# Kernel optimization log

Hardware: AMD Instinct MI355X
Metric: run time of the kernel (lower is better)

The kernel has to match this reference:

```python
import jax, jax.numpy as jnp
import numpy as np

ROUTING_ITER = 3
EPS = 1e-8


def squash(caps, axis=-1, eps=EPS):
    dot = jnp.sum(caps * caps, axis=axis, keepdims=True)
    scale = dot / (1.0 + dot) / jnp.sqrt(dot + eps)
    return scale * caps


def setup_inputs() -> dict:
    key = jax.random.key(0)
    k1, k2, k3 = jax.random.split(key, 3)
    B, I, O, D_in, D_out = 32, 1024, 64, 16, 32
    x = jax.random.normal(k1, (B, I, D_in), dtype=jnp.float32)
    W = jax.random.normal(k2, (1, I, O, D_out, D_in), dtype=jnp.float32) * 0.05
    b = jax.random.normal(k3, (1, 1, O, D_out), dtype=jnp.float32) * 0.05
    return {"x": x, "W": W, "b": b}


def reference(x, W, b):
    # u_hat[b,i,o,d] = sum_n W[0,i,o,d,n] * x[b,i,n]
    u_hat = jnp.einsum('iodn,bin->biod', W[0], x)  # [B, I, O, D_out]
    u_hat_det = jax.lax.stop_gradient(u_hat)
    B, I, O, _ = u_hat.shape
    b_ij = jnp.zeros((B, I, O, 1), dtype=x.dtype)
    v_j = None
    for it in range(ROUTING_ITER):
        c_ij = jax.nn.softmax(b_ij, axis=2)  # over output capsules
        if it == ROUTING_ITER - 1:
            s_j = jnp.sum(c_ij * u_hat, axis=1, keepdims=True) + b  # [B,1,O,D]
            v_j = squash(s_j, axis=-1)
        else:
            s_j = jnp.sum(c_ij * u_hat_det, axis=1, keepdims=True)
            v_j = squash(s_j, axis=-1)
            a_ij = jnp.sum(u_hat_det * v_j, axis=-1, keepdims=True)  # agreement
            b_ij = b_ij + a_ij
    return jnp.squeeze(v_j)  # [B, O, D_out]
```

## Files before the change

### kernel.cpp

```cpp
#include <hip/hip_runtime.h>
#include <hip/hip_bf16.h>
#include <stdint.h>

#define B_  32
#define I_  1024
#define O_  64
#define D_  32
#define N_  16
#define OD_ 2048

__device__ __forceinline__ uint32_t f2bf1(float f) {
  uint32_t u = __float_as_uint(f);
  return (u + 0x7fffu + ((u >> 16) & 1u)) >> 16;
}
__device__ __forceinline__ uint32_t pack2(float a, float b) {
  return f2bf1(a) | (f2bf1(b) << 16);
}
__device__ __forceinline__ float bflo(uint32_t v) { return __uint_as_float(v << 16); }
__device__ __forceinline__ float bfhi(uint32_t v) { return __uint_as_float(v & 0xffff0000u); }
__device__ __forceinline__ void unpack8(uint4 r, float* u) {
  u[0] = bflo(r.x); u[1] = bfhi(r.x);
  u[2] = bflo(r.y); u[3] = bfhi(r.y);
  u[4] = bflo(r.z); u[5] = bfhi(r.z);
  u[6] = bflo(r.w); u[7] = bfhi(r.w);
}

__global__ __launch_bounds__(256) void k_einsum(const float* __restrict__ x,
                                                const float* __restrict__ W,
                                                uint16_t* __restrict__ uhat) {
  const int i = blockIdx.x >> 2;
  const int q = blockIdx.x & 3;
  const int t = threadIdx.x;
  const int od0 = q * 512 + t;
  __shared__ float xs[B_ * N_];
  for (int e = t; e < B_ * N_; e += 256) {
    int bb = e >> 4, n = e & 15;
    xs[e] = x[(size_t)bb * (I_ * N_) + (size_t)i * N_ + n];
  }
  float wA[16], wB[16];
  {
    const float4* Wa = (const float4*)(W + (size_t)i * (OD_ * N_) + (size_t)od0 * N_);
    const float4* Wb = (const float4*)(W + (size_t)i * (OD_ * N_) + (size_t)(od0 + 256) * N_);
    #pragma unroll
    for (int qq = 0; qq < 4; ++qq) {
      float4 fa = Wa[qq];
      wA[qq * 4 + 0] = fa.x; wA[qq * 4 + 1] = fa.y;
      wA[qq * 4 + 2] = fa.z; wA[qq * 4 + 3] = fa.w;
      float4 fb = Wb[qq];
      wB[qq * 4 + 0] = fb.x; wB[qq * 4 + 1] = fb.y;
      wB[qq * 4 + 2] = fb.z; wB[qq * 4 + 3] = fb.w;
    }
  }
  __syncthreads();
  #pragma unroll 2
  for (int bb = 0; bb < B_; ++bb) {
    float4 x0 = ((const float4*)(xs + bb * 16))[0];
    float4 x1 = ((const float4*)(xs + bb * 16))[1];
    float4 x2 = ((const float4*)(xs + bb * 16))[2];
    float4 x3 = ((const float4*)(xs + bb * 16))[3];
    float xv[16] = {x0.x, x0.y, x0.z, x0.w, x1.x, x1.y, x1.z, x1.w,
                    x2.x, x2.y, x2.z, x2.w, x3.x, x3.y, x3.z, x3.w};
    float a0 = 0.f, a1 = 0.f;
    #pragma unroll
    for (int n = 0; n < 16; ++n) {
      a0 = fmaf(wA[n], xv[n], a0);
      a1 = fmaf(wB[n], xv[n], a1);
    }
    const size_t base = ((size_t)bb * I_ + i) * OD_ + od0;
    uhat[base]       = (uint16_t)f2bf1(a0);
    uhat[base + 256] = (uint16_t)f2bf1(a1);
  }
}

__global__ __launch_bounds__(256) void k_sum0(const uint4* __restrict__ uhat,
                                              uint4* __restrict__ part) {
  const int b = blockIdx.x >> 5, chunk = blockIdx.x & 31;
  const int t = threadIdx.x;
  float acc[8] = {0.f, 0.f, 0.f, 0.f, 0.f, 0.f, 0.f, 0.f};
  const size_t ubase = (((size_t)b * I_ + (size_t)chunk * 32) * OD_ + (size_t)t * 8) >> 3;
  #pragma unroll 8
  for (int ii = 0; ii < 32; ++ii) {
    uint4 r = uhat[ubase + (size_t)ii * (OD_ / 8)];
    float u[8]; unpack8(r, u);
    #pragma unroll
    for (int j = 0; j < 8; ++j) acc[j] += u[j];
  }
  part[(((size_t)b * 32 + chunk) * OD_ + (size_t)t * 8) >> 3] =
      make_uint4(pack2(acc[0], acc[1]), pack2(acc[2], acc[3]),
                 pack2(acc[4], acc[5]), pack2(acc[6], acc[7]));
}

__global__ __launch_bounds__(256) void k_squash(const uint16_t* __restrict__ part,
                                                const float* __restrict__ bias,
                                                float* __restrict__ vout,
                                                float scale, int addBias) {
  const int lane = threadIdx.x & 63;
  const int row = blockIdx.x * 4 + (threadIdx.x >> 6);
  const int b = row >> 6, o = row & 63;
  const int d = lane & 31;
  const uint16_t* p = part + (size_t)b * (32 * OD_) + (size_t)o * 32 + d;
  float s = 0.f;
  const int c0 = (lane >> 5) * 16;
  for (int c = c0; c < c0 + 16; ++c)
    s += __uint_as_float(((uint32_t)p[(size_t)c * OD_]) << 16);
  s += __shfl_xor(s, 32);
  s *= scale;
  if (addBias) s += bias[o * 32 + d];
  float dot = s * s;
  #pragma unroll
  for (int off = 1; off <= 16; off <<= 1) dot += __shfl_xor(dot, off);
  float sc = dot / (1.f + dot) / sqrtf(dot + 1e-8f);
  if (lane < 32) vout[(size_t)row * 32 + d] = s * sc;
}

__global__ __launch_bounds__(256) void k_route(const uint4* __restrict__ uhat,
                                               const float* __restrict__ vprev,
                                               float* __restrict__ bij,
                                               uint4* __restrict__ part,
                                               int secondIter) {
  const int b = blockIdx.x >> 5, chunk = blockIdx.x & 31;
  const int t = threadIdx.x;
  const int w = t >> 6, lane = t & 63;
  __shared__ float red[4][64][32];
  uint32_t vp[16];
  {
    const float4* vpt = (const float4*)(vprev + ((size_t)b * 64 + lane) * 32);
    #pragma unroll
    for (int q = 0; q < 8; ++q) {
      float4 f = vpt[q];
      vp[2 * q]     = pack2(f.x, f.y);
      vp[2 * q + 1] = pack2(f.z, f.w);
    }
  }
  float s_acc[32];
  #pragma unroll
  for (int d = 0; d < 32; ++d) s_acc[d] = 0.f;
  const int i0 = chunk * 32 + w * 8;
  const uint4* ub = uhat + ((size_t)b * I_ + i0) * 256 + (size_t)lane * 4;
  for (int r = 0; r < 8; ++r) {
    const uint4* uc = ub + (size_t)r * 256;
    uint4 c0 = uc[0], c1 = uc[1], c2 = uc[2], c3 = uc[3];
    float a = 0.f;
    {
      float u8[8];
      unpack8(c0, u8);
      #pragma unroll
      for (int p = 0; p < 4; ++p) {
        uint32_t vv = vp[p];
        a = fmaf(u8[2 * p], bflo(vv), a);
        a = fmaf(u8[2 * p + 1], bfhi(vv), a);
      }
      unpack8(c1, u8);
      #pragma unroll
      for (int p = 0; p < 4; ++p) {
        uint32_t vv = vp[4 + p];
        a = fmaf(u8[2 * p], bflo(vv), a);
        a = fmaf(u8[2 * p + 1], bfhi(vv), a);
      }
      unpack8(c2, u8);
      #pragma unroll
      for (int p = 0; p < 4; ++p) {
        uint32_t vv = vp[8 + p];
        a = fmaf(u8[2 * p], bflo(vv), a);
        a = fmaf(u8[2 * p + 1], bfhi(vv), a);
      }
      unpack8(c3, u8);
      #pragma unroll
      for (int p = 0; p < 4; ++p) {
        uint32_t vv = vp[12 + p];
        a = fmaf(u8[2 * p], bflo(vv), a);
        a = fmaf(u8[2 * p + 1], bfhi(vv), a);
      }
    }
    const int i = i0 + r;
    const size_t bidx = ((size_t)b * I_ + i) * 64 + lane;
    float bn = a;
    if (secondIter) bn += bij[bidx];
    else            bij[bidx] = bn;
    float m = bn;
    #pragma unroll
    for (int off = 1; off <= 32; off <<= 1) m = fmaxf(m, __shfl_xor(m, off));
    float e = __expf(bn - m);
    float sm = e;
    #pragma unroll
    for (int off = 1; off <= 32; off <<= 1) sm += __shfl_xor(sm, off);
    const float c = e / sm;
    {
      float u8[8];
      unpack8(c0, u8);
      #pragma unroll
      for (int j = 0; j < 8; ++j) s_acc[j] = fmaf(c, u8[j], s_acc[j]);
      unpack8(c1, u8);
      #pragma unroll
      for (int j = 0; j < 8; ++j) s_acc[8 + j] = fmaf(c, u8[j], s_acc[8 + j]);
      unpack8(c2, u8);
      #pragma unroll
      for (int j = 0; j < 8; ++j) s_acc[16 + j] = fmaf(c, u8[j], s_acc[16 + j]);
      unpack8(c3, u8);
      #pragma unroll
      for (int j = 0; j < 8; ++j) s_acc[24 + j] = fmaf(c, u8[j], s_acc[24 + j]);
    }
  }
  #pragma unroll
  for (int d = 0; d < 32; ++d) red[w][lane][(d + lane) & 31] = s_acc[d];
  __syncthreads();
  {
    const int o = t >> 2, db = (t & 3) * 8;
    float sum[8];
    #pragma unroll
    for (int j = 0; j < 8; ++j) {
      const int sw = (db + j + o) & 31;
      sum[j] = red[0][o][sw] + red[1][o][sw] + red[2][o][sw] + red[3][o][sw];
    }
    part[(((size_t)b * 32 + chunk) * OD_ + (size_t)t * 8) >> 3] =
        make_uint4(pack2(sum[0], sum[1]), pack2(sum[2], sum[3]),
                   pack2(sum[4], sum[5]), pack2(sum[6], sum[7]));
  }
}

extern "C" void kernel_launch(void* const* d_in, const int* in_sizes, int n_in,
                              void* d_out, int out_size, void* d_ws, size_t ws_size,
                              hipStream_t stream) {
  const float* x    = (const float*)d_in[0];
  const float* W    = (const float*)d_in[1];
  const float* bias = (const float*)d_in[2];
  float* out = (float*)d_out;

  char* ws = (char*)d_ws;
  uint16_t* uhat1 = (uint16_t*)ws;
  uint4*    uhat4 = (uint4*)ws;
  float* bij  = (float*)(ws + 134217728ull);
  uint4* part = (uint4*)(ws + 134217728ull + 8388608ull);
  uint16_t* part16 = (uint16_t*)part;
  float* vbuf = (float*)(ws + 134217728ull + 8388608ull + 4194304ull);

  k_einsum<<<dim3(I_ * 4), dim3(256), 0, stream>>>(x, W, uhat1);
  k_sum0  <<<dim3(1024), dim3(256), 0, stream>>>(uhat4, part);
  k_squash<<<dim3(512),  dim3(256), 0, stream>>>(part16, bias, vbuf, 1.f / 64.f, 0);
  k_route <<<dim3(1024), dim3(256), 0, stream>>>(uhat4, vbuf, bij, part, 0);
  k_squash<<<dim3(512),  dim3(256), 0, stream>>>(part16, bias, vbuf, 1.f, 0);
  k_route <<<dim3(1024), dim3(256), 0, stream>>>(uhat4, vbuf, bij, part, 1);
  k_squash<<<dim3(512),  dim3(256), 0, stream>>>(part16, bias, out, 1.f, 1);
}
```

Baseline: 297.2 us.

## Fuse first-iteration capsule sum into the einsum kernel and drop k_sum0

The einsum kernel now also accumulates the per-batch sum over a chunk of 8 input capsules and writes bf16 partial sums, so the separate k_sum0 pass that re-read the whole u_hat tensor is removed. The block mapping changes: each block covers 8 input capsules and 256 output columns, loading x for those capsules into shared memory and streaming W per capsule. Squash gains a chunk-count parameter to reduce 128 partials for the first iteration. This trades a full 128 MB re-read for a larger partial buffer and 32 accumulator registers per thread, and W loads are no longer spread across as many blocks.

```diff
diff --git a/kernel.cpp b/kernel.cpp
--- a/kernel.cpp
+++ b/kernel.cpp
@@ -25,83 +25,74 @@
   u[6] = bflo(r.w); u[7] = bfhi(r.w);
 }
 
-__global__ __launch_bounds__(256) void k_einsum(const float* __restrict__ x,
-                                                const float* __restrict__ W,
-                                                uint16_t* __restrict__ uhat) {
-  const int i = blockIdx.x >> 2;
-  const int q = blockIdx.x & 3;
-  const int t = threadIdx.x;
-  const int od0 = q * 512 + t;
-  __shared__ float xs[B_ * N_];
-  for (int e = t; e < B_ * N_; e += 256) {
-    int bb = e >> 4, n = e & 15;
-    xs[e] = x[(size_t)bb * (I_ * N_) + (size_t)i * N_ + n];
-  }
-  float wA[16], wB[16];
-  {
-    const float4* Wa = (const float4*)(W + (size_t)i * (OD_ * N_) + (size_t)od0 * N_);
-    const float4* Wb = (const float4*)(W + (size_t)i * (OD_ * N_) + (size_t)(od0 + 256) * N_);
-    #pragma unroll
-    for (int qq = 0; qq < 4; ++qq) {
-      float4 fa = Wa[qq];
-      wA[qq * 4 + 0] = fa.x; wA[qq * 4 + 1] = fa.y;
-      wA[qq * 4 + 2] = fa.z; wA[qq * 4 + 3] = fa.w;
-      float4 fb = Wb[qq];
-      wB[qq * 4 + 0] = fb.x; wB[qq * 4 + 1] = fb.y;
-      wB[qq * 4 + 2] = fb.z; wB[qq * 4 + 3] = fb.w;
-    }
+__global__ __launch_bounds__(256) void k_einsum_fused(const float* __restrict__ x,
+                                                      const float* __restrict__ W,
+                                                      uint16_t* __restrict__ uhat,
+                                                      uint16_t* __restrict__ parte) {
+  const int e  = blockIdx.x & 7;
+  const int ic = blockIdx.x >> 3;
+  const int t  = threadIdx.x;
+  const int od = e * 256 + t;
+  const int i0 = ic * 8;
+  __shared__ float xs[8 * 32 * 16];
+  for (int idx = t; idx < 8 * 32 * 16; idx += 256) {
+    int ii = idx >> 9, rem = idx & 511, bb = rem >> 4, n = rem & 15;
+    xs[idx] = x[(size_t)bb * (I_ * N_) + (size_t)(i0 + ii) * N_ + n];
   }
   __syncthreads();
-  #pragma unroll 2
-  for (int bb = 0; bb < B_; ++bb) {
-    float4 x0 = ((const float4*)(xs + bb * 16))[0];
-    float4 x1 = ((const float4*)(xs + bb * 16))[1];
-    float4 x2 = ((const float4*)(xs + bb * 16))[2];
-    float4 x3 = ((const float4*)(xs + bb * 16))[3];
-    float xv[16] = {x0.x, x0.y, x0.z, x0.w, x1.x, x1.y, x1.z, x1.w,
-                    x2.x, x2.y, x2.z, x2.w, x3.x, x3.y, x3.z, x3.w};
-    float a0 = 0.f, a1 = 0.f;
-    #pragma unroll
-    for (int n = 0; n < 16; ++n) {
-      a0 = fmaf(wA[n], xv[n], a0);
-      a1 = fmaf(wB[n], xv[n], a1);
-    }
-    const size_t base = ((size_t)bb * I_ + i) * OD_ + od0;
-    uhat[base]       = (uint16_t)f2bf1(a0);
-    uhat[base + 256] = (uint16_t)f2bf1(a1);
-  }
-}
-
-__global__ __launch_bounds__(256) void k_sum0(const uint4* __restrict__ uhat,
-                                              uint4* __restrict__ part) {
-  const int b = blockIdx.x >> 5, chunk = blockIdx.x & 31;
-  const int t = threadIdx.x;
-  float acc[8] = {0.f, 0.f, 0.f, 0.f, 0.f, 0.f, 0.f, 0.f};
-  const size_t ubase = (((size_t)b * I_ + (size_t)chunk * 32) * OD_ + (size_t)t * 8) >> 3;
-  #pragma unroll 8
-  for (int ii = 0; ii < 32; ++ii) {
-    uint4 r = uhat[ubase + (size_t)ii * (OD_ / 8)];
-    float u[8]; unpack8(r, u);
-    #pragma unroll
-    for (int j = 0; j < 8; ++j) acc[j] += u[j];
-  }
-  part[(((size_t)b * 32 + chunk) * OD_ + (size_t)t * 8) >> 3] =
-      make_uint4(pack2(acc[0], acc[1]), pack2(acc[2], acc[3]),
-                 pack2(acc[4], acc[5]), pack2(acc[6], acc[7]));
+  float sum_acc[32];
+  #pragma unroll
+  for (int bb = 0; bb < 32; ++bb) sum_acc[bb] = 0.f;
+  for (int ii = 0; ii < 8; ++ii) {
+    const int i = i0 + ii;
+    float w[16];
+    {
+      const float4* Wr = (const float4*)(W + (size_t)i * (OD_ * N_) + (size_t)od * N_);
+      #pragma unroll
+      for (int qq = 0; qq < 4; ++qq) {
+        float4 f = Wr[qq];
+        w[qq * 4 + 0] = f.x; w[qq * 4 + 1] = f.y;
+        w[qq * 4 + 2] = f.z; w[qq * 4 + 3] = f.w;
+      }
+    }
+    const float* xb = xs + ii * 512;
+    #pragma unroll 4
+    for (int bb = 0; bb < 32; ++bb) {
+      float4 x0 = ((const float4*)(xb + bb * 16))[0];
+      float4 x1 = ((const float4*)(xb + bb * 16))[1];
+      float4 x2 = ((const float4*)(xb + bb * 16))[2];
+      float4 x3 = ((const float4*)(xb + bb * 16))[3];
+      float a = 0.f;
+      a = fmaf(w[0],  x0.x, a); a = fmaf(w[1],  x0.y, a);
+      a = fmaf(w[2],  x0.z, a); a = fmaf(w[3],  x0.w, a);
+      a = fmaf(w[4],  x1.x, a); a = fmaf(w[5],  x1.y, a);
+      a = fmaf(w[6],  x1.z, a); a = fmaf(w[7],  x1.w, a);
+      a = fmaf(w[8],  x2.x, a); a = fmaf(w[9],  x2.y, a);
+      a = fmaf(w[10], x2.z, a); a = fmaf(w[11], x2.w, a);
+      a = fmaf(w[12], x3.x, a); a = fmaf(w[13], x3.y, a);
+      a = fmaf(w[14], x3.z, a); a = fmaf(w[15], x3.w, a);
+      uhat[((size_t)bb * I_ + i) * OD_ + od] = (uint16_t)f2bf1(a);
+      sum_acc[bb] += a;
+    }
+  }
+  #pragma unroll
+  for (int bb = 0; bb < 32; ++bb)
+    parte[((size_t)bb * 128 + ic) * OD_ + od] = (uint16_t)f2bf1(sum_acc[bb]);
 }
 
 __global__ __launch_bounds__(256) void k_squash(const uint16_t* __restrict__ part,
                                                 const float* __restrict__ bias,
                                                 float* __restrict__ vout,
-                                                float scale, int addBias) {
+                                                float scale, int addBias, int nchunk) {
   const int lane = threadIdx.x & 63;
   const int row = blockIdx.x * 4 + (threadIdx.x >> 6);
   const int b = row >> 6, o = row & 63;
   const int d = lane & 31;
-  const uint16_t* p = part + (size_t)b * (32 * OD_) + (size_t)o * 32 + d;
+  const uint16_t* p = part + (size_t)b * ((size_t)nchunk * OD_) + (size_t)o * 32 + d;
   float s = 0.f;
-  const int c0 = (lane >> 5) * 16;
-  for (int c = c0; c < c0 + 16; ++c)
+  const int half = nchunk >> 1;
+  const int c0 = (lane >> 5) * half;
+  for (int c = c0; c < c0 + half; ++c)
     s += __uint_as_float(((uint32_t)p[(size_t)c * OD_]) << 16);
   s += __shfl_xor(s, 32);
   s *= scale;
@@ -180,11 +171,11 @@
     float m = bn;
     #pragma unroll
     for (int off = 1; off <= 32; off <<= 1) m = fmaxf(m, __shfl_xor(m, off));
-    float e = __expf(bn - m);
-    float sm = e;
+    float ev = __expf(bn - m);
+    float sm = ev;
     #pragma unroll
     for (int off = 1; off <= 32; off <<= 1) sm += __shfl_xor(sm, off);
-    const float c = e / sm;
+    const float c = ev / sm;
     {
       float u8[8];
       unpack8(c0, u8);
@@ -229,16 +220,16 @@
   char* ws = (char*)d_ws;
   uint16_t* uhat1 = (uint16_t*)ws;
   uint4*    uhat4 = (uint4*)ws;
-  float* bij  = (float*)(ws + 134217728ull);
-  uint4* part = (uint4*)(ws + 134217728ull + 8388608ull);
-  uint16_t* part16 = (uint16_t*)part;
-  float* vbuf = (float*)(ws + 134217728ull + 8388608ull + 4194304ull);
-
-  k_einsum<<<dim3(I_ * 4), dim3(256), 0, stream>>>(x, W, uhat1);
-  k_sum0  <<<dim3(1024), dim3(256), 0, stream>>>(uhat4, part);
-  k_squash<<<dim3(512),  dim3(256), 0, stream>>>(part16, bias, vbuf, 1.f / 64.f, 0);
-  k_route <<<dim3(1024), dim3(256), 0, stream>>>(uhat4, vbuf, bij, part, 0);
-  k_squash<<<dim3(512),  dim3(256), 0, stream>>>(part16, bias, vbuf, 1.f, 0);
-  k_route <<<dim3(1024), dim3(256), 0, stream>>>(uhat4, vbuf, bij, part, 1);
-  k_squash<<<dim3(512),  dim3(256), 0, stream>>>(part16, bias, out, 1.f, 1);
-}
+  float* bij   = (float*)(ws + 134217728ull);
+  uint16_t* parte16 = (uint16_t*)(ws + 134217728ull + 8388608ull);
+  uint4*    partr4  = (uint4*)(ws + 134217728ull + 8388608ull);
+  uint16_t* partr16 = (uint16_t*)partr4;
+  float* vbuf = (float*)(ws + 134217728ull + 8388608ull + 16777216ull);
+
+  k_einsum_fused<<<dim3(1024), dim3(256), 0, stream>>>(x, W, uhat1, parte16);
+  k_squash<<<dim3(512), dim3(256), 0, stream>>>(parte16, bias, vbuf, 1.f / 64.f, 0, 128);
+  k_route <<<dim3(1024), dim3(256), 0, stream>>>(uhat4, vbuf, bij, partr4, 0);
+  k_squash<<<dim3(512), dim3(256), 0, stream>>>(partr16, bias, vbuf, 1.f, 0, 32);
+  k_route <<<dim3(1024), dim3(256), 0, stream>>>(uhat4, vbuf, bij, partr4, 1);
+  k_squash<<<dim3(512), dim3(256), 0, stream>>>(partr16, bias, out, 1.f, 1, 32);
+}
```

New measurement: 325.0 us. 1.09x slower.
